# Kernel tuning notes

Hardware: AMD Instinct MI355X
Metric: run time of the kernel (lower is better)

Reference implementation:

```python
import jax, jax.numpy as jnp
import numpy as np

N = 50000      # nodes
E = 500000     # edges
D = 128        # model dim (in_dim == out_dim)
H = 8          # heads
DH = D // H    # head dim = 16
BN_EPS = 1e-5
Z_EPS = 1e-6


def setup_inputs() -> dict:
    key = jax.random.key(0)
    ks = jax.random.split(key, 24)
    w = lambda k, shape, s=0.05: (jax.random.normal(k, shape, jnp.float32) * s)
    inp = {}
    inp['v'] = jax.random.normal(ks[0], (N, D), jnp.float32)
    inp['e'] = jax.random.normal(ks[1], (E, D), jnp.float32)
    inp['envelope'] = jax.random.uniform(ks[2], (E, 1, 1), jnp.float32)
    inp['src'] = jax.random.randint(ks[3], (E,), 0, N, jnp.int32)
    inp['dst'] = jax.random.randint(ks[4], (E,), 0, N, jnp.int32)
    # attention projections (use_bias=False)
    inp['WQ'] = w(ks[5], (D, D)); inp['WK'] = w(ks[6], (D, D))
    inp['WV'] = w(ks[7], (D, D)); inp['We'] = w(ks[8], (D, D))
    # output projections
    inp['WO_v'] = w(ks[9], (D, D)); inp['bO_v'] = jnp.zeros((D,), jnp.float32)
    inp['WO_e'] = w(ks[10], (D, D)); inp['bO_e'] = jnp.zeros((D,), jnp.float32)
    # batch-norm affine params
    inp['g1_v'] = jnp.ones((D,), jnp.float32); inp['b1_v'] = jnp.zeros((D,), jnp.float32)
    inp['g1_e'] = jnp.ones((D,), jnp.float32); inp['b1_e'] = jnp.zeros((D,), jnp.float32)
    inp['g2_v'] = jnp.ones((D,), jnp.float32); inp['b2_v'] = jnp.zeros((D,), jnp.float32)
    inp['g2_e'] = jnp.ones((D,), jnp.float32); inp['b2_e'] = jnp.zeros((D,), jnp.float32)
    # FFN weights (hidden = 2*D)
    inp['W1v'] = w(ks[11], (D, 2 * D)); inp['b1v'] = jnp.zeros((2 * D,), jnp.float32)
    inp['W2v'] = w(ks[12], (2 * D, D)); inp['b2v'] = jnp.zeros((D,), jnp.float32)
    inp['W1e'] = w(ks[13], (D, 2 * D)); inp['b1e'] = jnp.zeros((2 * D,), jnp.float32)
    inp['W2e'] = w(ks[14], (2 * D, D)); inp['b2e'] = jnp.zeros((D,), jnp.float32)
    return inp


def _batchnorm(x, g, b):
    # BatchNorm1d in training mode: biased batch stats over axis 0
    m = x.mean(0)
    var = x.var(0)
    return (x - m) * jax.lax.rsqrt(var + BN_EPS) * g + b


def _forward(v, e, envelope, src, dst,
             WQ, WK, WV, We, WO_v, bO_v, WO_e, bO_e,
             g1_v, b1_v, g1_e, b1_e,
             W1v, b1v, W2v, b2v, W1e, b1e, W2e, b2e,
             g2_v, b2_v, g2_e, b2_e):
    # --- multi-head edge attention ---
    Q = (v @ WQ).reshape(N, H, DH)
    K = (v @ WK).reshape(N, H, DH)
    V = (v @ WV).reshape(N, H, DH)
    pe = (e @ We).reshape(E, H, DH)
    # score = K[src] * Q[dst] / sqrt(Dh) * proj_e   (elementwise, per head)
    score = K[src] * Q[dst] / np.sqrt(DH).astype(np.float32) * pe  # [E,H,Dh]
    e_attn = score.reshape(E, D)                                    # e_out
    s = jnp.exp(jnp.clip(score.sum(-1, keepdims=True), -5.0, 5.0))  # [E,H,1]
    msg = V[src] * envelope * s                                     # [E,H,Dh]
    wV = jax.ops.segment_sum(msg, dst, num_segments=N)              # [N,H,Dh]
    z = jax.ops.segment_sum(s, dst, num_segments=N)                 # [N,H,1]
    v_attn = (wV / (z + Z_EPS)).reshape(N, D)
    # --- O projection + residual + batchnorm ---
    v1 = _batchnorm(v + (v_attn @ WO_v + bO_v), g1_v, b1_v)
    e1 = _batchnorm(e + (e_attn @ WO_e + bO_e), g1_e, b1_e)
    # --- FFN + residual + batchnorm ---
    v2 = _batchnorm(v1 + (jax.nn.relu(v1 @ W1v + b1v) @ W2v + b2v), g2_v, b2_v)
    e2 = _batchnorm(e1 + (jax.nn.relu(e1 @ W1e + b1e) @ W2e + b2e), g2_e, b2_e)
    return v2, e2


def reference(v, e, envelope, src, dst,
              WQ, WK, WV, We, WO_v, bO_v, WO_e, bO_e,
              g1_v, b1_v, g1_e, b1_e,
              W1v, b1v, W2v, b2v, W1e, b1e, W2e, b2e,
              g2_v, b2_v, g2_e, b2_e):
    return _forward(v, e, envelope, src, dst,
                    WQ, WK, WV, We, WO_v, bO_v, WO_e, bO_e,
                    g1_v, b1_v, g1_e, b1_e,
                    W1v, b1v, W2v, b2v, W1e, b1e, W2e, b2e,
                    g2_v, b2_v, g2_e, b2_e)
```

## Files before the change

### kernel.cpp

```cpp
#include <hip/hip_runtime.h>
#include <hip/hip_bf16.h>

#define N_NODES 50000
#define N_EDGES 500000
#define DIM 128
#define RSTRIDE 256

typedef __bf16 bf16_t;
typedef __bf16 bf16x8 __attribute__((ext_vector_type(8)));
typedef __bf16 bf16x4 __attribute__((ext_vector_type(4)));
typedef __bf16 bf16x2 __attribute__((ext_vector_type(2)));
typedef float f32x4 __attribute__((ext_vector_type(4)));

#define MFMA(a,b,c) __builtin_amdgcn_mfma_f32_16x16x32_bf16((a),(b),(c),0,0,0)

__device__ __forceinline__ int swz(int row, int kbyte){ return kbyte ^ ((row & 7) << 4); }
__device__ __forceinline__ int hswz(int row, int kbyte){ return kbyte ^ ((row & 15) << 4); }

__device__ __forceinline__ bf16x8 lds_frag(const char* s, int row, int rowb, int kbyte){
  return *(const bf16x8*)(s + row * rowb + swz(row, kbyte));
}

__device__ __forceinline__ void copy16(char* dst, const char* __restrict__ src, int bytes){
  for (int o = threadIdx.x * 16; o < bytes; o += blockDim.x * 16)
    *(f32x4*)(dst + o) = *(const f32x4*)(src + o);
}

struct WPrep {
  const float* w[10];
  int Kd[10], Nd[10], off[10], cum[10], mode[10];
};

__global__ void k_wprep(WPrep d, char* img, int total){
  for (int idx = blockIdx.x * blockDim.x + threadIdx.x; idx < total; idx += gridDim.x * blockDim.x){
    int i = 0;
#pragma unroll
    for (int j = 1; j < 10; j++) if (idx >= d.cum[j]) i = j;
    int loc = idx - d.cum[i];
    int K = d.Kd[i], N = d.Nd[i];
    int n = loc / K, k = loc - n * K;
    float val = d.w[i][(size_t)k * N + n];
    int nn = n;
    if (d.mode[i] == 1) nn = ((n & 7) << 4) | (n >> 3);
    if (d.mode[i] == 3) nn = ((n & 15) << 4) | (n >> 4);
    *(bf16_t*)(img + d.off[i] + nn * (K * 2) + swz(nn, k * 2)) = (bf16_t)val;
  }
}

__global__ void k_count(const int* __restrict__ dst, int* __restrict__ cnt){
  int i = blockIdx.x * blockDim.x + threadIdx.x;
  if (i < N_EDGES) atomicAdd(&cnt[dst[i]], 1);
}

__global__ __launch_bounds__(1024) void k_scan(const int* __restrict__ cnt,
                                               int* __restrict__ rowptr, int* __restrict__ wp){
  __shared__ int wsum[16];
  __shared__ int wpre[16];
  __shared__ int scarry;
  const int tid = threadIdx.x, lane = tid & 63, wv = tid >> 6;
  if (tid == 0) scarry = 0;
  for (int base = 0; base < N_NODES; base += 8192){
    int i0 = base + tid * 8;
    int v[8], p[8];
    int tsum = 0;
#pragma unroll
    for (int j = 0; j < 8; j++){
      int idx = i0 + j;
      v[j] = (idx < N_NODES) ? cnt[idx] : 0;
      p[j] = tsum; tsum += v[j];
    }
    int x = tsum;
#pragma unroll
    for (int off = 1; off < 64; off <<= 1){
      int t = __shfl_up(x, off);
      if (lane >= off) x += t;
    }
    if (lane == 63) wsum[wv] = x;
    __syncthreads();
    if (tid == 0){
      int run = scarry;
#pragma unroll
      for (int j = 0; j < 16; j++){ int t = wsum[j]; wpre[j] = run; run += t; }
      scarry = run;
    }
    __syncthreads();
    int texcl = wpre[wv] + x - tsum;
#pragma unroll
    for (int j = 0; j < 8; j++){
      int idx = i0 + j;
      if (idx < N_NODES){ rowptr[idx] = texcl + p[j]; wp[idx] = texcl + p[j]; }
    }
    __syncthreads();
  }
  if (tid == 0) rowptr[N_NODES] = scarry;
}

__global__ void k_fill(const int* __restrict__ dst, int* __restrict__ wp, int* __restrict__ csr){
  int i = blockIdx.x * blockDim.x + threadIdx.x;
  if (i < N_EDGES){
    int p = atomicAdd(&wp[dst[i]], 1);
    csr[p] = i;
  }
}

__global__ __launch_bounds__(512) void k_qkv(
    const float* __restrict__ v, const char* __restrict__ img,
    bf16_t* __restrict__ Q, bf16_t* __restrict__ K, bf16_t* __restrict__ V, int M)
{
  __shared__ __align__(16) char sm[65536];
  char* sX = sm;
  char* sW = sm + 32768;
  const int tid = threadIdx.x, lane = tid & 63, wave = tid >> 6;
  const int r0 = blockIdx.x * 128;
  for (int c = tid; c < 2048; c += 512){
    int row = c >> 4, kc = c & 15, grow = r0 + row;
    float f[8];
    if (grow < M){
      const float4* p = (const float4*)(v + (size_t)grow * DIM + kc * 8);
      float4 u0 = p[0], u1 = p[1];
      f[0]=u0.x; f[1]=u0.y; f[2]=u0.z; f[3]=u0.w;
      f[4]=u1.x; f[5]=u1.y; f[6]=u1.z; f[7]=u1.w;
    } else {
#pragma unroll
      for (int j=0;j<8;j++) f[j] = 0.f;
    }
    bf16x8 o;
#pragma unroll
    for (int j=0;j<8;j++) o[j] = (bf16_t)f[j];
    *(bf16x8*)(sX + row * 256 + swz(row, kc * 16)) = o;
  }
  const int rowA = wave * 16 + (lane & 15);
  const int kb0 = (lane >> 4) * 16;
  const int crow = wave*16 + (lane >> 4)*4;
  const int ccol = lane & 15;
  const f32x4 zero4 = {0.f, 0.f, 0.f, 0.f};
#pragma unroll
  for (int w3 = 0; w3 < 3; w3++){
    __syncthreads();
    copy16(sW, img + w3 * 32768, 32768);
    __syncthreads();
    f32x4 acc[8];
#pragma unroll
    for (int b=0;b<8;b++) acc[b] = zero4;
#pragma unroll
    for (int ks=0; ks<4; ks++){
      bf16x8 a = lds_frag(sX, rowA, 256, ks*64 + kb0);
#pragma unroll
      for (int nt=0; nt<8; nt++){
        int rn = nt*16 + (lane & 15);
        bf16x8 b = lds_frag(sW, rn, 256, ks*64 + kb0);
        acc[nt] = MFMA(a, b, acc[nt]);
      }
    }
    bf16_t* o = (w3 == 0) ? Q : ((w3 == 1) ? K : V);
#pragma unroll
    for (int r=0; r<4; r++){
      int grow = r0 + crow + r;
      if (grow < M){
        bf16x8 t;
#pragma unroll
        for (int nt=0; nt<8; nt++) t[nt] = (bf16_t)acc[nt][r];
        *(bf16x8*)(o + (size_t)grow * DIM + ccol*8) = t;
      }
    }
  }
}

__global__ __launch_bounds__(512, 4) void k_edge(
    const float* __restrict__ e,
    const int* __restrict__ src, const int* __restrict__ dst,
    const bf16_t* __restrict__ Qb, const bf16_t* __restrict__ Kb,
    const char* __restrict__ imgWe, const char* __restrict__ imgWo,
    const float* __restrict__ bOe,
    bf16_t* __restrict__ e1_pre, float* __restrict__ sv,
    float* __restrict__ stats, int M)
{
  __shared__ __align__(16) char sm[33792];
  char* sBuf = sm;
  float* sStats = (float*)(sm + 32768);
  const int tid = threadIdx.x, lane = tid & 63, wave = tid >> 6;
  const int r0 = blockIdx.x * 128;
  const int q = lane >> 4, ccol = lane & 15;
  const int crow = wave*16 + q*4;
  const int rowA = wave*16 + ccol;
  const int kb0 = q * 16;
  bf16x8 Kg[4], Qg[4];
#pragma unroll
  for (int r=0;r<4;r++){
    int ed = r0 + crow + r; if (ed >= M) ed = M - 1;
    int sn = src[ed], dn = dst[ed];
    Kg[r] = *(const bf16x8*)(Kb + (size_t)sn * DIM + ccol * 8);
    Qg[r] = *(const bf16x8*)(Qb + (size_t)dn * DIM + ccol * 8);
  }
  int grA = r0 + rowA; if (grA >= M) grA = M - 1;
  const f32x4* epA = (const f32x4*)(e + (size_t)grA * DIM);
  f32x4 ea[8];
#pragma unroll
  for (int ks=0; ks<4; ks++){
    ea[2*ks]   = epA[ks*8 + q*2];
    ea[2*ks+1] = epA[ks*8 + q*2 + 1];
  }
  copy16(sBuf, imgWe, 32768);
  bf16x8 eAb[4];
#pragma unroll
  for (int ks=0; ks<4; ks++){
#pragma unroll
    for (int j=0;j<4;j++){
      eAb[ks][j]   = (bf16_t)ea[2*ks][j];
      eAb[ks][4+j] = (bf16_t)ea[2*ks+1][j];
    }
  }
  __syncthreads();
  const f32x4 zero4 = {0.f,0.f,0.f,0.f};
  f32x4 pe[8];
#pragma unroll
  for (int i=0;i<8;i++) pe[i] = zero4;
#pragma unroll
  for (int ks=0; ks<4; ks++){
#pragma unroll
    for (int nt=0; nt<8; nt++){
      bf16x8 b = lds_frag(sBuf, nt*16 + ccol, 256, ks*64 + kb0);
      pe[nt] = MFMA(eAb[ks], b, pe[nt]);
    }
  }
  __syncthreads();
#pragma unroll
  for (int r=0;r<4;r++){
    int row = crow + r;
    bf16x8 t;
    float hsum = 0.f;
#pragma unroll
    for (int nt=0; nt<8; nt++){
      float sc = pe[nt][r] * 0.25f * (float)Kg[r][nt] * (float)Qg[r][nt];
      t[nt] = (bf16_t)sc;
      hsum += sc;
    }
    *(bf16x8*)(sBuf + row*256 + swz(row, ccol*16)) = t;
    float ts = hsum + __shfl_xor(hsum, 1);
    int ed = r0 + row;
    if (!(ccol & 1) && ed < M)
      sv[(size_t)ed*8 + (ccol >> 1)] = __expf(fminf(5.f, fmaxf(-5.f, ts)));
  }
  bf16x8 w2a[4];
#pragma unroll
  for (int ks=0; ks<4; ks++)
    w2a[ks] = *(const bf16x8*)(imgWo + rowA*256 + swz(rowA, ks*64 + kb0));
  __syncthreads();
  f32x4 a2[8];
#pragma unroll
  for (int i=0;i<8;i++) a2[i] = zero4;
#pragma unroll
  for (int ks=0; ks<4; ks++){
#pragma unroll
    for (int nt=0; nt<8; nt++){
      bf16x8 b = lds_frag(sBuf, nt*16 + ccol, 256, ks*64 + kb0);
      a2[nt] = MFMA(w2a[ks], b, a2[nt]);
    }
  }
  float4 bo = *(const float4*)(bOe + crow);
  float s1[4] = {0.f,0.f,0.f,0.f}, s2[4] = {0.f,0.f,0.f,0.f};
#pragma unroll
  for (int nt=0; nt<8; nt++){
    int erow = r0 + nt*16 + ccol;
    int gr = (erow < M) ? erow : (M - 1);
    f32x4 er = *(const f32x4*)(e + (size_t)gr*DIM + crow);
    float val[4];
    val[0] = a2[nt][0] + er[0] + bo.x;
    val[1] = a2[nt][1] + er[1] + bo.y;
    val[2] = a2[nt][2] + er[2] + bo.z;
    val[3] = a2[nt][3] + er[3] + bo.w;
    if (erow < M){
      bf16x4 t;
#pragma unroll
      for (int r=0;r<4;r++) t[r] = (bf16_t)val[r];
      *(bf16x4*)(e1_pre + (size_t)erow*RSTRIDE + crow) = t;
    } else {
#pragma unroll
      for (int r=0;r<4;r++) val[r] = 0.f;
    }
#pragma unroll
    for (int r=0;r<4;r++){ s1[r] += val[r]; s2[r] += val[r]*val[r]; }
  }
#pragma unroll
  for (int r=0;r<4;r++){
    s1[r] += __shfl_xor(s1[r], 1); s1[r] += __shfl_xor(s1[r], 2);
    s1[r] += __shfl_xor(s1[r], 4); s1[r] += __shfl_xor(s1[r], 8);
    s2[r] += __shfl_xor(s2[r], 1); s2[r] += __shfl_xor(s2[r], 2);
    s2[r] += __shfl_xor(s2[r], 4); s2[r] += __shfl_xor(s2[r], 8);
  }
  if (ccol == 0){
#pragma unroll
    for (int r=0;r<4;r++){
      sStats[crow + r] = s1[r];
      sStats[128 + crow + r] = s2[r];
    }
  }
  __syncthreads();
  if (tid < 256) unsafeAtomicAdd(&stats[tid], sStats[tid]);
}

__global__ __launch_bounds__(512) void k_agg(
    const int* __restrict__ rowptr, const int* __restrict__ csr,
    const int* __restrict__ src, const float* __restrict__ envl,
    const float* __restrict__ sv, const bf16_t* __restrict__ V,
    bf16_t* __restrict__ vAttn, int M)
{
  const int wave = threadIdx.x >> 6, lane = threadIdx.x & 63;
  const int n = blockIdx.x * 8 + wave;
  if (n >= M) return;
  const int beg = rowptr[n], end = rowptr[n + 1];
  const int h = lane >> 3;
  float ax = 0.f, ay = 0.f, zacc = 0.f;
  int i = beg;
  for (; i + 4 <= end; i += 4){
    int e0 = csr[i], e1 = csr[i+1], e2 = csr[i+2], e3 = csr[i+3];
    int sn0 = src[e0], sn1 = src[e1], sn2 = src[e2], sn3 = src[e3];
    float sv0 = sv[(size_t)e0*8 + h], sv1 = sv[(size_t)e1*8 + h];
    float sv2 = sv[(size_t)e2*8 + h], sv3 = sv[(size_t)e3*8 + h];
    float n0 = envl[e0], n1 = envl[e1], n2 = envl[e2], n3 = envl[e3];
    bf16x2 a0 = *(const bf16x2*)(V + (size_t)sn0 * DIM + lane * 2);
    bf16x2 a1 = *(const bf16x2*)(V + (size_t)sn1 * DIM + lane * 2);
    bf16x2 a2v = *(const bf16x2*)(V + (size_t)sn2 * DIM + lane * 2);
    bf16x2 a3 = *(const bf16x2*)(V + (size_t)sn3 * DIM + lane * 2);
    float w0 = n0*sv0, w1 = n1*sv1, w2 = n2*sv2, w3 = n3*sv3;
    ax += (float)a0[0]*w0 + (float)a1[0]*w1 + (float)a2v[0]*w2 + (float)a3[0]*w3;
    ay += (float)a0[1]*w0 + (float)a1[1]*w1 + (float)a2v[1]*w2 + (float)a3[1]*w3;
    zacc += sv0 + sv1 + sv2 + sv3;
  }
  for (; i < end; i++){
    int eid = csr[i];
    int sn = src[eid];
    float s = sv[(size_t)eid * 8 + h];
    float env = envl[eid];
    const bf16x2 vv = *(const bf16x2*)(V + (size_t)sn * DIM + lane * 2);
    float w = env * s;
    ax += (float)vv[0] * w; ay += (float)vv[1] * w;
    zacc += s;
  }
  float inv = 1.f / (zacc + 1e-6f);
  bf16x2 o; o[0] = (bf16_t)(ax * inv); o[1] = (bf16_t)(ay * inv);
  *(bf16x2*)(vAttn + (size_t)n * DIM + lane * 2) = o;
}

__global__ __launch_bounds__(512) void k_nodeout(
    const bf16_t* __restrict__ vAttn, const float* __restrict__ v,
    const char* __restrict__ imgWo, const float* __restrict__ bOv,
    bf16_t* __restrict__ v1_pre, float* __restrict__ stats, int M)
{
  __shared__ __align__(16) char sm[66560];
  char* sW = sm;
  char* sX = sm + 32768;
  float* sStats = (float*)(sm + 65536);
  const int tid = threadIdx.x, lane = tid & 63, wave = tid >> 6;
  const int r0 = blockIdx.x * 128;
  copy16(sW, imgWo, 32768);
  if (tid < 256) sStats[tid] = 0.f;
  for (int c = tid; c < 2048; c += 512){
    int row = c >> 4, kc = c & 15, grow = r0 + row;
    bf16x8 o;
    if (grow < M){
      o = *(const bf16x8*)(vAttn + (size_t)grow * DIM + kc * 8);
    } else {
#pragma unroll
      for (int j=0;j<8;j++) o[j] = (bf16_t)0.f;
    }
    *(bf16x8*)(sX + row*256 + swz(row, kc*16)) = o;
  }
  __syncthreads();
  const int rowA = wave*16 + (lane & 15);
  const int kb0 = (lane >> 4)*16;
  const f32x4 zero4 = {0.f,0.f,0.f,0.f};
  f32x4 acc[8];
#pragma unroll
  for (int i=0;i<8;i++) acc[i]=zero4;
#pragma unroll
  for (int ks=0;ks<4;ks++){
    bf16x8 a = lds_frag(sX, rowA, 256, ks*64+kb0);
#pragma unroll
    for (int nt=0;nt<8;nt++){
      int rn = nt*16 + (lane&15);
      bf16x8 b = lds_frag(sW, rn, 256, ks*64+kb0);
      acc[nt] = MFMA(a,b,acc[nt]);
    }
  }
  const int crow = wave*16 + (lane>>4)*4;
  const int ccol = lane & 15;
  float4 bo0 = *(const float4*)(bOv + ccol*8);
  float4 bo1 = *(const float4*)(bOv + ccol*8 + 4);
  float s1[8], s2[8];
#pragma unroll
  for (int j=0;j<8;j++){ s1[j]=0.f; s2[j]=0.f; }
#pragma unroll
  for (int r=0;r<4;r++){
    int grow = r0 + crow + r;
    float val[8];
    if (grow < M){
      const float4* vp = (const float4*)(v + (size_t)grow*DIM + ccol*8);
      float4 v0 = vp[0], v1 = vp[1];
      val[0]=acc[0][r]+v0.x+bo0.x; val[1]=acc[1][r]+v0.y+bo0.y;
      val[2]=acc[2][r]+v0.z+bo0.z; val[3]=acc[3][r]+v0.w+bo0.w;
      val[4]=acc[4][r]+v1.x+bo1.x; val[5]=acc[5][r]+v1.y+bo1.y;
      val[6]=acc[6][r]+v1.z+bo1.z; val[7]=acc[7][r]+v1.w+bo1.w;
      bf16x8 t;
#pragma unroll
      for (int j=0;j<8;j++) t[j] = (bf16_t)val[j];
      *(bf16x8*)(v1_pre + (size_t)grow*RSTRIDE + ccol*8) = t;
    } else {
#pragma unroll
      for (int j=0;j<8;j++) val[j]=0.f;
    }
#pragma unroll
    for (int j=0;j<8;j++){ s1[j] += val[j]; s2[j] += val[j]*val[j]; }
  }
#pragma unroll
  for (int j=0;j<8;j++){
    s1[j] += __shfl_xor(s1[j], 16); s1[j] += __shfl_xor(s1[j], 32);
    s2[j] += __shfl_xor(s2[j], 16); s2[j] += __shfl_xor(s2[j], 32);
  }
  if (lane < 16){
#pragma unroll
    for (int j=0;j<8;j++){
      atomicAdd(&sStats[ccol*8 + j], s1[j]);
      atomicAdd(&sStats[128 + ccol*8 + j], s2[j]);
    }
  }
  __syncthreads();
  if (tid < 256) unsafeAtomicAdd(&stats[tid], sStats[tid]);
}

struct FinArgs { const float* st; const float* g; const float* b; float* ss; float invM; };

__global__ void k_finstats(FinArgs a0, FinArgs a1){
  FinArgs a = (blockIdx.x == 0) ? a0 : a1;
  int c = threadIdx.x;
  float mean = a.st[c] * a.invM;
  float var  = a.st[128 + c] * a.invM - mean * mean;
  float scl  = a.g[c] * rsqrtf(var + 1e-5f);
  a.ss[c] = scl;
  a.ss[128 + c] = a.b[c] - mean * scl;
}

__global__ __launch_bounds__(512, 6) void k_ffn(
    bf16_t* __restrict__ xio, const float* __restrict__ ss1,
    const char* __restrict__ img1, const float* __restrict__ b1,
    const char* __restrict__ img2, const float* __restrict__ b2,
    float* __restrict__ stats2, int M)
{
  __shared__ __align__(16) char sm[33792];
  char* sBuf = sm;
  float* sStats = (float*)(sm + 32768);
  const int tid = threadIdx.x, lane = tid & 63, wave = tid >> 6;
  const int r0 = blockIdx.x * 128;
  const int q = lane >> 4, ccol = lane & 15;
  const int kb0 = q * 16;
  const int crow = wave*16 + q*4;
  const int rowA = wave*16 + ccol;
  const f32x4 zero4 = {0.f,0.f,0.f,0.f};

  copy16(sBuf, img1, 32768);
  int grA = r0 + rowA; if (grA >= M) grA = M - 1;
  const bf16_t* xrow = xio + (size_t)grA * RSTRIDE;
  bf16x8 araw[4];
#pragma unroll
  for (int ks=0; ks<4; ks++)
    araw[ks] = *(const bf16x8*)(xrow + ks*32 + q*8);
  bf16x8 xAb[4];
#pragma unroll
  for (int ks=0; ks<4; ks++){
    const f32x4* sp = (const f32x4*)(ss1 + ks*32 + q*8);
    const f32x4* hp = (const f32x4*)(ss1 + 128 + ks*32 + q*8);
    f32x4 s0 = sp[0], s1v = sp[1], h0 = hp[0], h1 = hp[1];
#pragma unroll
    for (int j=0;j<4;j++){
      xAb[ks][j]   = (bf16_t)((float)araw[ks][j]  *s0[j]  + h0[j]);
      xAb[ks][4+j] = (bf16_t)((float)araw[ks][4+j]*s1v[j] + h1[j]);
    }
  }
  __syncthreads();

  bf16x8 hreg0[4], hreg1[4];
  f32x4 wbuf[4];
#pragma unroll
  for (int i=0;i<4;i++) wbuf[i] = *(const f32x4*)(img1 + 32768 + tid*16 + i*8192);
  {
    float4 bq0 = *(const float4*)(b1 + ccol*16);
    float4 bq1 = *(const float4*)(b1 + ccol*16 + 4);
    f32x4 acc[8];
#pragma unroll
    for (int i=0;i<8;i++) acc[i]=zero4;
#pragma unroll
    for (int ks=0;ks<4;ks++){
#pragma unroll
      for (int nt=0;nt<8;nt++){
        bf16x8 b = lds_frag(sBuf, nt*16 + ccol, 256, ks*64+kb0);
        acc[nt] = MFMA(xAb[ks], b, acc[nt]);
      }
    }
#pragma unroll
    for (int r=0;r<4;r++){
      bf16x8 t;
      t[0]=(bf16_t)fmaxf(acc[0][r]+bq0.x,0.f); t[1]=(bf16_t)fmaxf(acc[1][r]+bq0.y,0.f);
      t[2]=(bf16_t)fmaxf(acc[2][r]+bq0.z,0.f); t[3]=(bf16_t)fmaxf(acc[3][r]+bq0.w,0.f);
      t[4]=(bf16_t)fmaxf(acc[4][r]+bq1.x,0.f); t[5]=(bf16_t)fmaxf(acc[5][r]+bq1.y,0.f);
      t[6]=(bf16_t)fmaxf(acc[6][r]+bq1.z,0.f); t[7]=(bf16_t)fmaxf(acc[7][r]+bq1.w,0.f);
      hreg0[r] = t;
    }
  }
  __syncthreads();
#pragma unroll
  for (int i=0;i<4;i++) *(f32x4*)(sBuf + tid*16 + i*8192) = wbuf[i];
  __syncthreads();
  {
    float4 bq2 = *(const float4*)(b1 + ccol*16 + 8);
    float4 bq3 = *(const float4*)(b1 + ccol*16 + 12);
    f32x4 acc[8];
#pragma unroll
    for (int i=0;i<8;i++) acc[i]=zero4;
#pragma unroll
    for (int ks=0;ks<4;ks++){
#pragma unroll
      for (int nt=0;nt<8;nt++){
        bf16x8 b = lds_frag(sBuf, nt*16 + ccol, 256, ks*64+kb0);
        acc[nt] = MFMA(xAb[ks], b, acc[nt]);
      }
    }
#pragma unroll
    for (int r=0;r<4;r++){
      bf16x8 t;
      t[0]=(bf16_t)fmaxf(acc[0][r]+bq2.x,0.f); t[1]=(bf16_t)fmaxf(acc[1][r]+bq2.y,0.f);
      t[2]=(bf16_t)fmaxf(acc[2][r]+bq2.z,0.f); t[3]=(bf16_t)fmaxf(acc[3][r]+bq2.w,0.f);
      t[4]=(bf16_t)fmaxf(acc[4][r]+bq3.x,0.f); t[5]=(bf16_t)fmaxf(acc[5][r]+bq3.y,0.f);
      t[6]=(bf16_t)fmaxf(acc[6][r]+bq3.z,0.f); t[7]=(bf16_t)fmaxf(acc[7][r]+bq3.w,0.f);
      hreg1[r] = t;
    }
  }
  __syncthreads();

  if ((ccol >> 3) == 0){
    int cb = (ccol & 7) * 32;
#pragma unroll
    for (int r=0;r<4;r++){
      int row = crow + r;
      *(bf16x8*)(sBuf + row*256 + hswz(row, cb))      = hreg0[r];
      *(bf16x8*)(sBuf + row*256 + hswz(row, cb + 16)) = hreg1[r];
    }
  }
  __syncthreads();

  f32x4 o2[8];
#pragma unroll
  for (int i=0;i<8;i++) o2[i]=zero4;
  {
    bf16x8 w2a[4];
#pragma unroll
    for (int ks=0; ks<4; ks++)
      w2a[ks] = *(const bf16x8*)(img2 + (size_t)rowA*512 + swz(rowA, ks*64 + kb0));
#pragma unroll
    for (int ks=0; ks<4; ks++){
#pragma unroll
      for (int nt=0; nt<8; nt++){
        int m = nt*16 + ccol;
        bf16x8 b = *(const bf16x8*)(sBuf + m*256 + hswz(m, ks*64 + kb0));
        o2[nt] = MFMA(w2a[ks], b, o2[nt]);
      }
    }
  }
  __syncthreads();
  if ((ccol >> 3) == 1){
    int cb = (ccol & 7) * 32;
#pragma unroll
    for (int r=0;r<4;r++){
      int row = crow + r;
      *(bf16x8*)(sBuf + row*256 + hswz(row, cb))      = hreg0[r];
      *(bf16x8*)(sBuf + row*256 + hswz(row, cb + 16)) = hreg1[r];
    }
  }
  __syncthreads();
  {
    bf16x8 w2a[4];
#pragma unroll
    for (int ks=0; ks<4; ks++)
      w2a[ks] = *(const bf16x8*)(img2 + (size_t)rowA*512 + swz(rowA, 256 + ks*64 + kb0));
#pragma unroll
    for (int ks=0; ks<4; ks++){
#pragma unroll
      for (int nt=0; nt<8; nt++){
        int m = nt*16 + ccol;
        bf16x8 b = *(const bf16x8*)(sBuf + m*256 + hswz(m, ks*64 + kb0));
        o2[nt] = MFMA(w2a[ks], b, o2[nt]);
      }
    }
  }

  float4 ssc = *(const float4*)(ss1 + crow);
  float4 ssh = *(const float4*)(ss1 + 128 + crow);
  float4 b2v = *(const float4*)(b2 + crow);
  float s1[4] = {0.f,0.f,0.f,0.f}, s2[4] = {0.f,0.f,0.f,0.f};
#pragma unroll
  for (int nt=0; nt<8; nt++){
    int erow = r0 + nt*16 + ccol;
    int gr = (erow < M) ? erow : (M - 1);
    bf16x4 u = *(const bf16x4*)(xio + (size_t)gr*RSTRIDE + crow);
    float val[4];
    val[0] = (float)u[0]*ssc.x + ssh.x + o2[nt][0] + b2v.x;
    val[1] = (float)u[1]*ssc.y + ssh.y + o2[nt][1] + b2v.y;
    val[2] = (float)u[2]*ssc.z + ssh.z + o2[nt][2] + b2v.z;
    val[3] = (float)u[3]*ssc.w + ssh.w + o2[nt][3] + b2v.w;
    if (erow < M){
      bf16x4 t;
#pragma unroll
      for (int r=0;r<4;r++) t[r] = (bf16_t)val[r];
      *(bf16x4*)(xio + (size_t)erow*RSTRIDE + crow) = t;
    } else {
#pragma unroll
      for (int r=0;r<4;r++) val[r] = 0.f;
    }
#pragma unroll
    for (int r=0;r<4;r++){ s1[r] += val[r]; s2[r] += val[r]*val[r]; }
  }
#pragma unroll
  for (int r=0;r<4;r++){
    s1[r] += __shfl_xor(s1[r], 1); s1[r] += __shfl_xor(s1[r], 2);
    s1[r] += __shfl_xor(s1[r], 4); s1[r] += __shfl_xor(s1[r], 8);
    s2[r] += __shfl_xor(s2[r], 1); s2[r] += __shfl_xor(s2[r], 2);
    s2[r] += __shfl_xor(s2[r], 4); s2[r] += __shfl_xor(s2[r], 8);
  }
  if (ccol == 0){
#pragma unroll
    for (int r=0;r<4;r++){
      sStats[crow + r] = s1[r];
      sStats[128 + crow + r] = s2[r];
    }
  }
  __syncthreads();
  if (tid < 256) unsafeAtomicAdd(&stats2[tid], sStats[tid]);
}

struct NormP { const float* st; const float* g; const float* bn; float invM; };

__global__ __launch_bounds__(256) void k_norm2(
    char* __restrict__ xv, char* __restrict__ xe,
    NormP pv, NormP pe, long long nv, long long ne)
{
  __shared__ float sSS[512];
  const int tid = threadIdx.x;
  {
    int side = tid >> 7, c = tid & 127;
    NormP pp = side ? pe : pv;
    float mean = pp.st[c] * pp.invM;
    float var  = pp.st[128 + c] * pp.invM - mean * mean;
    float scl  = pp.g[c] * rsqrtf(var + 1e-5f);
    sSS[side*256 + c] = scl;
    sSS[side*256 + 128 + c] = pp.bn[c] - mean * scl;
  }
  __syncthreads();
  long long tv = nv * 16, total = tv + ne * 16;
  for (long long g = (long long)blockIdx.x * blockDim.x + tid; g < total;
       g += (long long)gridDim.x * blockDim.x){
    bool isv = g < tv;
    char* base = isv ? xv : xe;
    const float* ss = isv ? sSS : (sSS + 256);
    long long gg = isv ? g : g - tv;
    long long row = gg >> 4;
    int c = (int)(gg & 15);
    bf16x8 u = *(const bf16x8*)(base + row * 512 + c * 16);
    int c0 = c * 8;
    float4 o0, o1;
    o0.x = (float)u[0]*ss[c0+0] + ss[128+c0+0];
    o0.y = (float)u[1]*ss[c0+1] + ss[128+c0+1];
    o0.z = (float)u[2]*ss[c0+2] + ss[128+c0+2];
    o0.w = (float)u[3]*ss[c0+3] + ss[128+c0+3];
    o1.x = (float)u[4]*ss[c0+4] + ss[128+c0+4];
    o1.y = (float)u[5]*ss[c0+5] + ss[128+c0+5];
    o1.z = (float)u[6]*ss[c0+6] + ss[128+c0+6];
    o1.w = (float)u[7]*ss[c0+7] + ss[128+c0+7];
    float4* dp = (float4*)(base + row * 512 + c * 32);
    dp[0] = o0; dp[1] = o1;
  }
}

extern "C" void kernel_launch(void* const* d_in, const int* in_sizes, int n_in,
                              void* d_out, int out_size, void* d_ws, size_t ws_size,
                              hipStream_t stream)
{
  const float* v    = (const float*)d_in[0];
  const float* e    = (const float*)d_in[1];
  const float* envl = (const float*)d_in[2];
  const int*   src  = (const int*)d_in[3];
  const int*   dst  = (const int*)d_in[4];
  const float* bOv  = (const float*)d_in[10];
  const float* bOe  = (const float*)d_in[12];
  const float* g1v  = (const float*)d_in[13];
  const float* b1vn = (const float*)d_in[14];
  const float* g1e  = (const float*)d_in[15];
  const float* b1en = (const float*)d_in[16];
  const float* g2v  = (const float*)d_in[17];
  const float* b2vn = (const float*)d_in[18];
  const float* g2e  = (const float*)d_in[19];
  const float* b2en = (const float*)d_in[20];
  const float* b1vf = (const float*)d_in[22];
  const float* b2vf = (const float*)d_in[24];
  const float* b1ef = (const float*)d_in[26];
  const float* b2ef = (const float*)d_in[28];

  float* out_v = (float*)d_out;
  float* out_e = out_v + (size_t)N_NODES * DIM;
  bf16_t* v1b = (bf16_t*)out_v;
  bf16_t* e1b = (bf16_t*)out_e;

  char* ws = (char*)d_ws;
  const size_t IMG_OFF = 0;
  const size_t QB_OFF  = 458752;
  const size_t KB_OFF  = QB_OFF  + 12800000;
  const size_t VB_OFF  = KB_OFF  + 12800000;
  const size_t VA_OFF  = VB_OFF  + 12800000;
  const size_t SV_OFF  = VA_OFF  + 12800000;
  const size_t CSR_OFF = SV_OFF  + 16000000;
  const size_t RP_OFF  = CSR_OFF + 2000000;
  const size_t WP_OFF  = RP_OFF  + 200016;
  const size_t CNT_OFF = WP_OFF  + 200000;
  const size_t ST_OFF  = CNT_OFF + 200000;
  const size_t SS_OFF  = ST_OFF  + 4096;

  char*   img   = ws + IMG_OFF;
  bf16_t* Qb    = (bf16_t*)(ws + QB_OFF);
  bf16_t* Kb    = (bf16_t*)(ws + KB_OFF);
  bf16_t* Vb    = (bf16_t*)(ws + VB_OFF);
  bf16_t* vAttn = (bf16_t*)(ws + VA_OFF);
  float*  svp   = (float*)(ws + SV_OFF);
  int*    csr   = (int*)(ws + CSR_OFF);
  int*    rowp  = (int*)(ws + RP_OFF);
  int*    wpp   = (int*)(ws + WP_OFF);
  int*    cnt   = (int*)(ws + CNT_OFF);
  float*  st    = (float*)(ws + ST_OFF);
  float*  ssb   = (float*)(ws + SS_OFF);
  float* st_e1 = st;        float* st_v1 = st + 256;
  float* st_v2 = st + 512;  float* st_e2 = st + 768;
  float* ss_v1 = ssb;       float* ss_e1 = ssb + 256;

  (void)hipMemsetAsync(ws + CNT_OFF, 0, 200000 + 4096, stream);

  WPrep wp;
  const int wid[10]   = {5,6,7,8,9,11,21,23,25,27};
  const int Ks[10]    = {128,128,128,128,128,128,128,256,128,256};
  const int Ns[10]    = {128,128,128,128,128,128,256,128,256,128};
  const int modes[10] = {1,1,1,1,1,0,3,0,3,0};
  int cum = 0, off = 0;
  for (int i = 0; i < 10; i++){
    wp.w[i] = (const float*)d_in[wid[i]];
    wp.Kd[i] = Ks[i]; wp.Nd[i] = Ns[i];
    wp.off[i] = off; wp.cum[i] = cum; wp.mode[i] = modes[i];
    off += Ks[i]*Ns[i]*2; cum += Ks[i]*Ns[i];
  }
  k_wprep<<<896, 256, 0, stream>>>(wp, img, cum);

  k_count<<<1954, 256, 0, stream>>>(dst, cnt);
  k_scan<<<1, 1024, 0, stream>>>(cnt, rowp, wpp);
  k_fill<<<1954, 256, 0, stream>>>(dst, wpp, csr);

  k_qkv<<<391, 512, 0, stream>>>(v, img, Qb, Kb, Vb, N_NODES);

  k_edge<<<3907, 512, 0, stream>>>(e, src, dst, Qb, Kb,
                                   img + 98304 , img + 163840 , bOe,
                                   e1b, svp, st_e1, N_EDGES);

  k_agg<<<6250, 512, 0, stream>>>(rowp, csr, src, envl, svp, Vb, vAttn, N_NODES);

  k_nodeout<<<391, 512, 0, stream>>>(vAttn, v, img + 131072 , bOv,
                                     v1b, st_v1, N_NODES);

  {
    FinArgs fv{st_v1, g1v, b1vn, ss_v1, 1.f / N_NODES};
    FinArgs fe{st_e1, g1e, b1en, ss_e1, 1.f / N_EDGES};
    k_finstats<<<2, 128, 0, stream>>>(fv, fe);
  }

  k_ffn<<<391, 512, 0, stream>>>(v1b, ss_v1, img + 196608 , b1vf,
                                 img + 262144 , b2vf, st_v2, N_NODES);
  k_ffn<<<3907, 512, 0, stream>>>(e1b, ss_e1, img + 327680 , b1ef,
                                  img + 393216 , b2ef, st_e2, N_EDGES);

  NormP npv{st_v2, g2v, b2vn, 1.f / N_NODES};
  NormP npe{st_e2, g2e, b2en, 1.f / N_EDGES};
  k_norm2<<<4096, 256, 0, stream>>>((char*)out_v, (char*)out_e, npv, npe,
                                    (long long)N_NODES, (long long)N_EDGES);
}
```

Measured before the change: 759.4 us.

## Relayout FFN hidden weights and stage output through LDS for row-contiguous epilogue

Changes the W1 column permutation so each 128-wide hidden half maps to contiguous column groups, which lets the hidden-tile LDS store be written by all lanes at once instead of half the lanes per pass. The FFN output is then transposed through LDS so each thread reads and writes 8 contiguous bf16 values per row of the residual stream rather than 4-element strided chunks. The batch-norm statistics reduction switches to shared-memory atomics across waves. This removes scattered 8-byte global accesses in the epilogue at the cost of an extra LDS round trip and two more barriers.

```diff
diff --git a/kernel.cpp b/kernel.cpp
--- a/kernel.cpp
+++ b/kernel.cpp
@@ -42,7 +42,7 @@
     float val = d.w[i][(size_t)k * N + n];
     int nn = n;
     if (d.mode[i] == 1) nn = ((n & 7) << 4) | (n >> 3);
-    if (d.mode[i] == 3) nn = ((n & 15) << 4) | (n >> 4);
+    if (d.mode[i] == 4){ int w7 = n & 127; nn = ((n >> 7) << 7) | ((w7 & 7) << 4) | (w7 >> 3); }
     *(bf16_t*)(img + d.off[i] + nn * (K * 2) + swz(nn, k * 2)) = (bf16_t)val;
   }
 }
@@ -458,6 +458,7 @@
   const f32x4 zero4 = {0.f,0.f,0.f,0.f};
 
   copy16(sBuf, img1, 32768);
+  if (tid < 256) sStats[tid] = 0.f;
   int grA = r0 + rowA; if (grA >= M) grA = M - 1;
   const bf16_t* xrow = xio + (size_t)grA * RSTRIDE;
   bf16x8 araw[4];
@@ -483,8 +484,8 @@
 #pragma unroll
   for (int i=0;i<4;i++) wbuf[i] = *(const f32x4*)(img1 + 32768 + tid*16 + i*8192);
   {
-    float4 bq0 = *(const float4*)(b1 + ccol*16);
-    float4 bq1 = *(const float4*)(b1 + ccol*16 + 4);
+    float4 bq0 = *(const float4*)(b1 + ccol*8);
+    float4 bq1 = *(const float4*)(b1 + ccol*8 + 4);
     f32x4 acc[8];
 #pragma unroll
     for (int i=0;i<8;i++) acc[i]=zero4;
@@ -511,8 +512,8 @@
   for (int i=0;i<4;i++) *(f32x4*)(sBuf + tid*16 + i*8192) = wbuf[i];
   __syncthreads();
   {
-    float4 bq2 = *(const float4*)(b1 + ccol*16 + 8);
-    float4 bq3 = *(const float4*)(b1 + ccol*16 + 12);
+    float4 bq2 = *(const float4*)(b1 + 128 + ccol*8);
+    float4 bq3 = *(const float4*)(b1 + 128 + ccol*8 + 4);
     f32x4 acc[8];
 #pragma unroll
     for (int i=0;i<8;i++) acc[i]=zero4;
@@ -536,14 +537,10 @@
   }
   __syncthreads();
 
-  if ((ccol >> 3) == 0){
-    int cb = (ccol & 7) * 32;
-#pragma unroll
-    for (int r=0;r<4;r++){
-      int row = crow + r;
-      *(bf16x8*)(sBuf + row*256 + hswz(row, cb))      = hreg0[r];
-      *(bf16x8*)(sBuf + row*256 + hswz(row, cb + 16)) = hreg1[r];
-    }
+#pragma unroll
+  for (int r=0;r<4;r++){
+    int row = crow + r;
+    *(bf16x8*)(sBuf + row*256 + hswz(row, ccol*16)) = hreg0[r];
   }
   __syncthreads();
 
@@ -566,14 +563,10 @@
     }
   }
   __syncthreads();
-  if ((ccol >> 3) == 1){
-    int cb = (ccol & 7) * 32;
-#pragma unroll
-    for (int r=0;r<4;r++){
-      int row = crow + r;
-      *(bf16x8*)(sBuf + row*256 + hswz(row, cb))      = hreg0[r];
-      *(bf16x8*)(sBuf + row*256 + hswz(row, cb + 16)) = hreg1[r];
-    }
+#pragma unroll
+  for (int r=0;r<4;r++){
+    int row = crow + r;
+    *(bf16x8*)(sBuf + row*256 + hswz(row, ccol*16)) = hreg1[r];
   }
   __syncthreads();
   {
@@ -591,45 +584,63 @@
       }
     }
   }
-
-  float4 ssc = *(const float4*)(ss1 + crow);
-  float4 ssh = *(const float4*)(ss1 + 128 + crow);
-  float4 b2v = *(const float4*)(b2 + crow);
-  float s1[4] = {0.f,0.f,0.f,0.f}, s2[4] = {0.f,0.f,0.f,0.f};
+  __syncthreads();
+
 #pragma unroll
   for (int nt=0; nt<8; nt++){
-    int erow = r0 + nt*16 + ccol;
-    int gr = (erow < M) ? erow : (M - 1);
-    bf16x4 u = *(const bf16x4*)(xio + (size_t)gr*RSTRIDE + crow);
-    float val[4];
-    val[0] = (float)u[0]*ssc.x + ssh.x + o2[nt][0] + b2v.x;
-    val[1] = (float)u[1]*ssc.y + ssh.y + o2[nt][1] + b2v.y;
-    val[2] = (float)u[2]*ssc.z + ssh.z + o2[nt][2] + b2v.z;
-    val[3] = (float)u[3]*ssc.w + ssh.w + o2[nt][3] + b2v.w;
-    if (erow < M){
-      bf16x4 t;
-#pragma unroll
-      for (int r=0;r<4;r++) t[r] = (bf16_t)val[r];
-      *(bf16x4*)(xio + (size_t)erow*RSTRIDE + crow) = t;
+    int m = nt*16 + ccol;
+    bf16x4 t;
+#pragma unroll
+    for (int r=0;r<4;r++) t[r] = (bf16_t)o2[nt][r];
+    *(bf16x4*)(sBuf + m*256 + swz(m, crow*2)) = t;
+  }
+  __syncthreads();
+
+  float4 sc0 = *(const float4*)(ss1 + ccol*8);
+  float4 sc1 = *(const float4*)(ss1 + ccol*8 + 4);
+  float4 sh0 = *(const float4*)(ss1 + 128 + ccol*8);
+  float4 sh1 = *(const float4*)(ss1 + 128 + ccol*8 + 4);
+  float4 b20 = *(const float4*)(b2 + ccol*8);
+  float4 b21 = *(const float4*)(b2 + ccol*8 + 4);
+  float s1[8], s2[8];
+#pragma unroll
+  for (int j=0;j<8;j++){ s1[j]=0.f; s2[j]=0.f; }
+#pragma unroll
+  for (int r=0;r<4;r++){
+    int row = crow + r, grow = r0 + row;
+    float val[8];
+    if (grow < M){
+      bf16x8 u = *(const bf16x8*)(xio + (size_t)grow*RSTRIDE + ccol*8);
+      bf16x8 ob = *(const bf16x8*)(sBuf + row*256 + swz(row, ccol*16));
+      val[0]=(float)u[0]*sc0.x+sh0.x + (float)ob[0]+b20.x;
+      val[1]=(float)u[1]*sc0.y+sh0.y + (float)ob[1]+b20.y;
+      val[2]=(float)u[2]*sc0.z+sh0.z + (float)ob[2]+b20.z;
+      val[3]=(float)u[3]*sc0.w+sh0.w + (float)ob[3]+b20.w;
+      val[4]=(float)u[4]*sc1.x+sh1.x + (float)ob[4]+b21.x;
+      val[5]=(float)u[5]*sc1.y+sh1.y + (float)ob[5]+b21.y;
+      val[6]=(float)u[6]*sc1.z+sh1.z + (float)ob[6]+b21.z;
+      val[7]=(float)u[7]*sc1.w+sh1.w + (float)ob[7]+b21.w;
+      bf16x8 t;
+#pragma unroll
+      for (int j=0;j<8;j++) t[j] = (bf16_t)val[j];
+      *(bf16x8*)(xio + (size_t)grow*RSTRIDE + ccol*8) = t;
     } else {
 #pragma unroll
-      for (int r=0;r<4;r++) val[r] = 0.f;
-    }
-#pragma unroll
-    for (int r=0;r<4;r++){ s1[r] += val[r]; s2[r] += val[r]*val[r]; }
-  }
-#pragma unroll
-  for (int r=0;r<4;r++){
-    s1[r] += __shfl_xor(s1[r], 1); s1[r] += __shfl_xor(s1[r], 2);
-    s1[r] += __shfl_xor(s1[r], 4); s1[r] += __shfl_xor(s1[r], 8);
-    s2[r] += __shfl_xor(s2[r], 1); s2[r] += __shfl_xor(s2[r], 2);
-    s2[r] += __shfl_xor(s2[r], 4); s2[r] += __shfl_xor(s2[r], 8);
-  }
-  if (ccol == 0){
-#pragma unroll
-    for (int r=0;r<4;r++){
-      sStats[crow + r] = s1[r];
-      sStats[128 + crow + r] = s2[r];
+      for (int j=0;j<8;j++) val[j]=0.f;
+    }
+#pragma unroll
+    for (int j=0;j<8;j++){ s1[j] += val[j]; s2[j] += val[j]*val[j]; }
+  }
+#pragma unroll
+  for (int j=0;j<8;j++){
+    s1[j] += __shfl_xor(s1[j], 16); s1[j] += __shfl_xor(s1[j], 32);
+    s2[j] += __shfl_xor(s2[j], 16); s2[j] += __shfl_xor(s2[j], 32);
+  }
+  if (lane < 16){
+#pragma unroll
+    for (int j=0;j<8;j++){
+      atomicAdd(&sStats[ccol*8 + j], s1[j]);
+      atomicAdd(&sStats[128 + ccol*8 + j], s2[j]);
     }
   }
   __syncthreads();
@@ -744,7 +755,7 @@
   const int wid[10]   = {5,6,7,8,9,11,21,23,25,27};
   const int Ks[10]    = {128,128,128,128,128,128,128,256,128,256};
   const int Ns[10]    = {128,128,128,128,128,128,256,128,256,128};
-  const int modes[10] = {1,1,1,1,1,0,3,0,3,0};
+  const int modes[10] = {1,1,1,1,1,0,4,0,4,0};
   int cum = 0, off = 0;
   for (int i = 0; i < 10; i++){
     wp.w[i] = (const float*)d_in[wid[i]];
```

Result: faster. 734.0 us (-3.3%).
